# Optimization experiments

Hardware: AMD Instinct MI355X
Metric: run time of the kernel (lower is better)

Reference implementation:

```python
import jax, jax.numpy as jnp
import numpy as np

B, S, E, H = 4, 512, 512, 8
DH = E // H
HID = max(16, E // 4)  # sr_ratio=4
ALPHA = 0.1
EPS_SAFE = 0.05  # eps=1e-6 clamped to [0.05, 0.8]


def _xavier(k, shape):
    fan_out, fan_in = shape[0], shape[1]
    lim = (6.0 / (fan_in + fan_out)) ** 0.5
    return jax.random.uniform(k, shape, minval=-lim, maxval=lim, dtype=jnp.float32)


def setup_inputs() -> dict:
    key = jax.random.key(0)
    ks = jax.random.split(key, 8)
    return {
        "x": jax.random.normal(ks[0], (B, S, E), dtype=jnp.float32),
        "wq": _xavier(ks[1], (E, E)), "bq": jnp.zeros((E,), jnp.float32),
        "wk": _xavier(ks[2], (E, E)), "bk": jnp.zeros((E,), jnp.float32),
        "wv": _xavier(ks[3], (E, E)), "bv": jnp.zeros((E,), jnp.float32),
        "wo": _xavier(ks[4], (E, E)), "bo": jnp.zeros((E,), jnp.float32),
        # sr_conv1: Conv2d(1, HID, 1) -> weight [HID,1,1,1] == vector [HID]
        "w1": _xavier(ks[5], (HID, 1)).reshape(HID), "b1": jnp.zeros((HID,), jnp.float32),
        # sr_conv2: Conv2d(HID, 1, 1) -> weight [1,HID,1,1] == vector [HID]
        "w2": _xavier(ks[6], (1, HID)).reshape(HID), "b2": jnp.zeros((), jnp.float32),
    }


def _autopoietic_transform(scores, w1, b1, w2, b2):
    # scores: [B, H, S, S]
    scores = jnp.clip(jnp.nan_to_num(scores, nan=0.0, posinf=10.0, neginf=-10.0), -15.0, 15.0)
    mean_attn = scores.mean(axis=1)  # mean over heads -> [B, S, S]

    scaled = jnp.clip(jnp.clip(mean_attn, -8.0, 8.0) * EPS_SAFE, -10.0, 10.0)
    # conv1x1 (1 -> HID): broadcastmul; clamp + relu; conv1x1 (HID -> 1)
    hid = scaled[:, None, :, :] * w1[None, :, None, None] + b1[None, :, None, None]  # [B,HID,S,S]
    hid = jax.nn.relu(jnp.clip(hid, -5.0, 5.0))
    auto = jnp.einsum('bhij,h->bij', hid, w2) + b2  # [B,S,S]
    auto = jnp.clip(auto, -5.0, 5.0)

    # Taylor expansion with clamp, then sigmoid smoothing
    taylor = jnp.clip(1.0 + 0.05 * (auto * 50.0), 0.5, 1.5)
    sig = jax.nn.sigmoid(taylor)

    # fuzzy probability via entropy of softmax of mean attention
    p = jax.nn.softmax(jnp.clip(mean_attn, -10.0, 10.0), axis=-1)
    Hent = -p * jnp.log(p + 1e-6)
    Fm = jax.nn.softmax(3.0 * Hent, axis=-1)

    t = sig * Fm

    # energy (Frobenius-norm) balancing per batch
    e_o = jnp.sqrt((mean_attn ** 2).sum(axis=(1, 2))) + 1e-4
    e_t = jnp.sqrt((t ** 2).sum(axis=(1, 2))) + 1e-4
    gamma = jnp.clip(e_o / e_t, 0.8, 1.2)[:, None, None]
    t = gamma * t

    # dynamic std matching
    t_mean = t.mean(axis=(1, 2), keepdims=True)
    o_mean = mean_attn.mean(axis=(1, 2), keepdims=True)
    t_std = jnp.sqrt(jnp.clip(((t - t_mean) ** 2).mean(axis=(1, 2), keepdims=True), 0.01, None))
    o_std = jnp.sqrt(jnp.clip(((mean_attn - o_mean) ** 2).mean(axis=(1, 2), keepdims=True), 0.01, None))
    gdyn = jnp.clip(o_std / t_std, 0.8, 1.2)
    t = o_mean + gdyn * (t - t_mean)

    # residual blend of transformed map back into per-head scores (alpha=0.1), final clamp
    return jnp.clip(scores + ALPHA * t[:, None, :, :], -15.0, 15.0)


def reference(x, wq, bq, wk, bk, wv, bv, wo, bo, w1, b1, w2, b2):
    scaling = DH ** -0.5
    q = (jnp.einsum('bse,oe->bso', x, wq) + bq).reshape(B, S, H, DH).transpose(0, 2, 1, 3) * scaling
    k = (jnp.einsum('bse,oe->bso', x, wk) + bk).reshape(B, S, H, DH).transpose(0, 2, 1, 3)
    v = (jnp.einsum('bse,oe->bso', x, wv) + bv).reshape(B, S, H, DH).transpose(0, 2, 1, 3)
    scores = jnp.einsum('bhqd,bhkd->bhqk', q, k)  # [B,H,S,S]
    scores = _autopoietic_transform(scores, w1, b1, w2, b2)
    attn = jax.nn.softmax(scores, axis=-1)
    out = jnp.einsum('bhqk,bhkd->bhqd', attn, v).transpose(0, 2, 1, 3).reshape(B, S, E)
    return jnp.einsum('bse,oe->bso', out, wo) + bo
```

## Files before the change

kernel.cpp:

```cpp
#include <hip/hip_runtime.h>
#include <math.h>

#define BATCH 4
#define SEQ   512
#define EMB   512
#define NH    8
#define DHD   64
#define HIDN  128
#define ALPHA 0.1f
#define EPSS  0.05f

#define LUTN  2048
#define XMIN  (-0.4f)
#define XSTEP (0.8f / LUTN)

typedef __attribute__((ext_vector_type(8))) short  bf16x8;
typedef __attribute__((ext_vector_type(4))) float  f32x4;
#define MFMA(a,b,c) __builtin_amdgcn_mfma_f32_16x16x32_bf16((a),(b),(c),0,0,0)

__device__ __forceinline__ unsigned short f2bf(float f) {
    union { float f; unsigned u; } v; v.f = f;
    unsigned r = v.u + 0x7fffu + ((v.u >> 16) & 1u);
    return (unsigned short)(r >> 16);
}
__device__ __forceinline__ float bf2f(unsigned short h) {
    union { unsigned u; float f; } v; v.u = ((unsigned)h) << 16;
    return v.f;
}

__device__ __forceinline__ void async_lds16(const unsigned short* g, unsigned short* l) {
    __builtin_amdgcn_global_load_lds(
        (const __attribute__((address_space(1))) void*)g,
        (__attribute__((address_space(3))) void*)l, 16, 0, 0);
}

template<int KSTEPS, int UN>
__device__ __forceinline__ void gemm_core(
    const unsigned short* __restrict__ A, const unsigned short* __restrict__ B,
    int m0, int n0, unsigned short* sA, unsigned short* sB, f32x4 acc[2][4])
{
    const int K = KSTEPS * 32;
    const int tid = threadIdx.x, w = tid >> 6, lane = tid & 63;
    const int quad = lane >> 4, r = lane & 15;
    const int wm = w >> 1, wn = w & 1;
    const int lrow = lane >> 2, lc = lane & 3;
    const int sc = lc ^ (lrow & 3);
    const unsigned short* ag  = A + (long)(m0 + w * 16 + lrow) * K + sc * 8;
    const unsigned short* bg0 = B + (long)(n0 + w * 16 + lrow) * K + sc * 8;
    const unsigned short* bg1 = (UN == 4)
        ? B + (long)(n0 + (w + 4) * 16 + lrow) * K + sc * 8 : (const unsigned short*)0;
    unsigned short* dA  = sA + w * 512;
    unsigned short* dB0 = sB + w * 512;
    unsigned short* dB1 = sB + (w + 4) * 512;
    const int cs = quad ^ (r & 3);

    for (int s = 0; s < KSTEPS; s++) {
        const int k0 = s * 32;
        async_lds16(ag + k0, dA);
        async_lds16(bg0 + k0, dB0);
        if (UN == 4) async_lds16(bg1 + k0, dB1);
        __syncthreads();
        bf16x8 af[2], bf[4];
        #pragma unroll
        for (int t = 0; t < 2; t++)
            af[t] = *(const bf16x8*)(sA + (wm * 32 + t * 16 + r) * 32 + cs * 8);
        #pragma unroll
        for (int u = 0; u < UN; u++)
            bf[u] = *(const bf16x8*)(sB + (wn * UN * 16 + u * 16 + r) * 32 + cs * 8);
        #pragma unroll
        for (int t = 0; t < 2; t++)
            #pragma unroll
            for (int u = 0; u < UN; u++)
                acc[t][u] = MFMA(af[t], bf[u], acc[t][u]);
        __syncthreads();
    }
}

__global__ __launch_bounds__(256) void gemm_qkv(
    const unsigned short* __restrict__ x_ext, const unsigned short* __restrict__ w_ext,
    const float* __restrict__ bq, const float* __restrict__ bk, const float* __restrict__ bv,
    unsigned short* __restrict__ q_ext, unsigned short* __restrict__ k_ext,
    unsigned short* __restrict__ vT)
{
    __shared__ __align__(16) unsigned short sA[64 * 32];
    __shared__ __align__(16) unsigned short sB[128 * 32];
    __shared__ float sC[64 * 132];

    const int m0 = blockIdx.y * 64, n0 = blockIdx.x * 128;
    f32x4 acc[2][4] = {};
    gemm_core<48, 4>(x_ext, w_ext, m0, n0, sA, sB, acc);

    const int tid = threadIdx.x, w = tid >> 6, lane = tid & 63;
    const int quad = lane >> 4, r = lane & 15;
    const int wm = w >> 1, wn = w & 1;
    #pragma unroll
    for (int t = 0; t < 2; t++)
        #pragma unroll
        for (int u = 0; u < 4; u++)
            #pragma unroll
            for (int g = 0; g < 4; g++)
                sC[(wm * 32 + t * 16 + quad * 4 + g) * 132 + wn * 64 + u * 16 + r] = acc[t][u][g];
    __syncthreads();

    const int which = n0 >> 9;
    const int n0l = n0 & 511;
    const int h0 = n0l >> 6;
    const int b = m0 >> 9, s0 = m0 & 511;

    if (which < 2) {
        const float scl = (which == 0) ? 0.125f : 1.0f;
        const float* bias = (which == 0) ? bq : bk;
        unsigned* dst = (unsigned*)((which == 0) ? q_ext : k_ext);
        #pragma unroll
        for (int seg = 0; seg < 3; seg++) {
            const bool lo = (which == 0) ? (seg == 1) : (seg == 2);
            for (int it = 0; it < 16; it++) {
                const int idx = it * 256 + tid;
                const int row = idx >> 5;
                const int hl = row >> 6, sl = row & 63;
                const int jc = idx & 31;
                const int nc = hl * 64 + jc * 2;
                float v0 = (sC[sl * 132 + nc]     + bias[n0l + nc])     * scl;
                float v1 = (sC[sl * 132 + nc + 1] + bias[n0l + nc + 1]) * scl;
                unsigned short a0 = f2bf(v0), a1 = f2bf(v1);
                if (lo) { a0 = f2bf(v0 - bf2f(a0)); a1 = f2bf(v1 - bf2f(a1)); }
                const long orow = (long)(b * NH + h0 + hl) * SEQ + s0 + sl;
                dst[orow * 96 + seg * 32 + jc] = (unsigned)a0 | ((unsigned)a1 << 16);
            }
        }
    } else {
        unsigned* dst = (unsigned*)vT;
        for (int it = 0; it < 16; it++) {
            const int idx = it * 256 + tid;
            const int row = idx >> 5;
            const int hl = row >> 6, d = row & 63;
            const int jc = idx & 31;
            const int sl = jc * 2;
            const float bvv = bv[n0l + hl * 64 + d];
            const float v0 = sC[sl * 132 + hl * 64 + d] + bvv;
            const float v1 = sC[(sl + 1) * 132 + hl * 64 + d] + bvv;
            const long orow = (long)(b * NH + h0 + hl) * DHD + d;
            dst[orow * 256 + (s0 >> 1) + jc] = (unsigned)f2bf(v0) | ((unsigned)f2bf(v1) << 16);
        }
    }
}

__global__ __launch_bounds__(256) void gemm_scores(
    const unsigned short* __restrict__ q_ext, const unsigned short* __restrict__ k_ext,
    float* __restrict__ scores)
{
    __shared__ __align__(16) unsigned short sA[64 * 32];
    __shared__ __align__(16) unsigned short sB[128 * 32];
    const int z = blockIdx.z;
    const int m0 = blockIdx.y * 64, n0 = blockIdx.x * 128;
    f32x4 acc[2][4] = {};
    gemm_core<6, 4>(q_ext + (long)z * SEQ * 192, k_ext + (long)z * SEQ * 192,
                    m0, n0, sA, sB, acc);
    float* C = scores + (long)z * SEQ * SEQ;
    const int tid = threadIdx.x, w = tid >> 6, lane = tid & 63;
    const int quad = lane >> 4, r = lane & 15;
    const int wm = w >> 1, wn = w & 1;
    #pragma unroll
    for (int t = 0; t < 2; t++)
        #pragma unroll
        for (int u = 0; u < 4; u++)
            #pragma unroll
            for (int g = 0; g < 4; g++) {
                const int m = m0 + wm * 32 + t * 16 + quad * 4 + g;
                const int n = n0 + wn * 64 + u * 16 + r;
                C[(long)m * SEQ + n] = fminf(fmaxf(acc[t][u][g], -15.f), 15.f);
            }
}

__global__ __launch_bounds__(256) void gemm_attnv(
    const unsigned short* __restrict__ attn, const unsigned short* __restrict__ vT,
    unsigned short* __restrict__ otmp)
{
    __shared__ __align__(16) unsigned short sA[64 * 32];
    __shared__ __align__(16) unsigned short sB[64 * 32];
    __shared__ float sC[64 * 66];
    const int z = blockIdx.z;
    const int m0 = blockIdx.y * 64;
    f32x4 acc[2][4] = {};
    gemm_core<16, 2>(attn + (long)z * SEQ * SEQ, vT + (long)z * DHD * SEQ,
                     m0, 0, sA, sB, acc);
    const int tid = threadIdx.x, w = tid >> 6, lane = tid & 63;
    const int quad = lane >> 4, r = lane & 15;
    const int wm = w >> 1, wn = w & 1;
    #pragma unroll
    for (int t = 0; t < 2; t++)
        #pragma unroll
        for (int u = 0; u < 2; u++)
            #pragma unroll
            for (int g = 0; g < 4; g++)
                sC[(wm * 32 + t * 16 + quad * 4 + g) * 66 + wn * 32 + u * 16 + r] = acc[t][u][g];
    __syncthreads();
    const int b = z >> 3, h = z & 7;
    unsigned* dst = (unsigned*)otmp;
    for (int it = 0; it < 8; it++) {
        const int idx = it * 256 + tid;
        const int sr = idx >> 5, jc = idx & 31;
        const float v0 = sC[sr * 66 + jc * 2], v1 = sC[sr * 66 + jc * 2 + 1];
        dst[((long)(b * SEQ + m0 + sr)) * 256 + h * 32 + jc] =
            (unsigned)f2bf(v0) | ((unsigned)f2bf(v1) << 16);
    }
}

__global__ __launch_bounds__(256) void gemm_proj(
    const unsigned short* __restrict__ otmp, const unsigned short* __restrict__ woh,
    const float* __restrict__ bo, float* __restrict__ out)
{
    __shared__ __align__(16) unsigned short sA[64 * 32];
    __shared__ __align__(16) unsigned short sB[64 * 32];
    const int m0 = blockIdx.y * 64, n0 = blockIdx.x * 64;
    f32x4 acc[2][4] = {};
    gemm_core<16, 2>(otmp, woh, m0, n0, sA, sB, acc);
    const int tid = threadIdx.x, w = tid >> 6, lane = tid & 63;
    const int quad = lane >> 4, r = lane & 15;
    const int wm = w >> 1, wn = w & 1;
    #pragma unroll
    for (int t = 0; t < 2; t++)
        #pragma unroll
        for (int u = 0; u < 2; u++)
            #pragma unroll
            for (int g = 0; g < 4; g++) {
                const int m = m0 + wm * 32 + t * 16 + quad * 4 + g;
                const int n = n0 + wn * 32 + u * 16 + r;
                out[(long)m * EMB + n] = acc[t][u][g] + bo[n];
            }
}

__device__ __forceinline__ float blockReduceMax(float v, float* sred) {
    #pragma unroll
    for (int o = 32; o > 0; o >>= 1) v = fmaxf(v, __shfl_down(v, o));
    __syncthreads();
    if ((threadIdx.x & 63) == 0) sred[threadIdx.x >> 6] = v;
    __syncthreads();
    return fmaxf(fmaxf(sred[0], sred[1]), fmaxf(sred[2], sred[3]));
}
__device__ __forceinline__ float blockReduceSum(float v, float* sred) {
    #pragma unroll
    for (int o = 32; o > 0; o >>= 1) v += __shfl_down(v, o);
    __syncthreads();
    if ((threadIdx.x & 63) == 0) sred[threadIdx.x >> 6] = v;
    __syncthreads();
    return (sred[0] + sred[1]) + (sred[2] + sred[3]);
}

__global__ __launch_bounds__(256) void prep_kernel(
    const float* __restrict__ x,
    const float* __restrict__ wq, const float* __restrict__ wk,
    const float* __restrict__ wv, const float* __restrict__ wo,
    const float* __restrict__ w1, const float* __restrict__ b1,
    const float* __restrict__ w2, const float* __restrict__ b2,
    unsigned short* __restrict__ x_ext, unsigned short* __restrict__ w_ext,
    unsigned short* __restrict__ woh, float* __restrict__ lut)
{
    const int blk = blockIdx.x;
    if (blk < 9) {
        const int i = blk * 256 + threadIdx.x;
        if (i > LUTN) return;
        const float xv = XMIN + i * XSTEP;
        float a = 0.f;
        for (int h = 0; h < HIDN; h++) {
            float hv = xv * w1[h] + b1[h];
            hv = fminf(fmaxf(hv, -5.f), 5.f);
            hv = fmaxf(hv, 0.f);
            a += hv * w2[h];
        }
        a += b2[0];
        a = fminf(fmaxf(a, -5.f), 5.f);
        const float taylor = fminf(fmaxf(1.f + 2.5f * a, 0.5f), 1.5f);
        lut[i] = 1.f / (1.f + expf(-taylor));
        return;
    }
    const int i = (blk - 9) * 256 + threadIdx.x;
    if (i < 1048576) {
        const int m = i >> 9, k = i & 511;
        const float v = x[i];
        const unsigned short h = f2bf(v), l = f2bf(v - bf2f(h));
        const long bb = (long)m * 1536 + k;
        x_ext[bb] = h; x_ext[bb + 512] = l; x_ext[bb + 1024] = h;
    } else if (i < 1835008) {
        const int j = i - 1048576;
        const int n = j >> 9, k = j & 511;
        const float v = (j < 262144) ? wq[j] : (j < 524288 ? wk[j - 262144] : wv[j - 524288]);
        const unsigned short h = f2bf(v), l = f2bf(v - bf2f(h));
        const long bb = (long)n * 1536 + k;
        w_ext[bb] = h; w_ext[bb + 512] = h; w_ext[bb + 1024] = l;
    } else {
        const int j = i - 1835008;
        woh[j] = f2bf(wo[j]);
    }
}

__global__ __launch_bounds__(256) void transform_kernel(
    const float* __restrict__ scores,
    const float* __restrict__ lut,
    float* __restrict__ t0,
    float4* __restrict__ partials)
{
    const int r = blockIdx.x;
    const int b = r >> 9, i = r & 511;
    const int tid = threadIdx.x;

    __shared__ float slut[LUTN + 1];
    __shared__ float sred[4];

    for (int u = tid; u <= LUTN; u += 256) slut[u] = lut[u];

    const float* base = scores + (((long)(b * NH)) * SEQ + i) * SEQ;

    float mv[2], sigv[2], mclip[2];
    float lmax = -1e30f;
    __syncthreads();
    #pragma unroll
    for (int u = 0; u < 2; u++) {
        const int j = tid + u * 256;
        float s = 0.f;
        #pragma unroll
        for (int h = 0; h < NH; h++) s += base[(long)h * SEQ * SEQ + j];
        const float m = s * (1.0f / NH);
        mv[u] = m;
        const float x = fminf(fmaxf(m, -8.f), 8.f) * EPSS;
        float t = (x - XMIN) * (1.0f / XSTEP);
        int idx = (int)t;
        idx = idx < 0 ? 0 : (idx > LUTN - 1 ? LUTN - 1 : idx);
        const float frac = t - (float)idx;
        const float l0 = slut[idx], l1 = slut[idx + 1];
        sigv[u] = l0 + frac * (l1 - l0);
        const float mc = fminf(fmaxf(m, -10.f), 10.f);
        mclip[u] = mc;
        lmax = fmaxf(lmax, mc);
    }

    const float rmax = blockReduceMax(lmax, sred);
    float ex[2], lsum = 0.f;
    #pragma unroll
    for (int u = 0; u < 2; u++) { ex[u] = expf(mclip[u] - rmax); lsum += ex[u]; }
    const float rsum = blockReduceSum(lsum, sred);
    const float inv = 1.f / rsum;

    float hent[2], lmax2 = -1e30f;
    #pragma unroll
    for (int u = 0; u < 2; u++) {
        const float p = ex[u] * inv;
        const float he = -p * logf(p + 1e-6f);
        hent[u] = 3.f * he;
        lmax2 = fmaxf(lmax2, hent[u]);
    }
    const float rmax2 = blockReduceMax(lmax2, sred);
    float ex2[2], lsum2 = 0.f;
    #pragma unroll
    for (int u = 0; u < 2; u++) { ex2[u] = expf(hent[u] - rmax2); lsum2 += ex2[u]; }
    const float rsum2 = blockReduceSum(lsum2, sred);
    const float inv2 = 1.f / rsum2;

    float s_m = 0.f, s_m2 = 0.f, s_t = 0.f, s_t2 = 0.f;
    #pragma unroll
    for (int u = 0; u < 2; u++) {
        const int j = tid + u * 256;
        const float Fm = ex2[u] * inv2;
        const float tv = sigv[u] * Fm;
        t0[((long)b * SEQ + i) * SEQ + j] = tv;
        s_m += mv[u]; s_m2 += mv[u] * mv[u];
        s_t += tv;    s_t2 += tv * tv;
    }
    s_m  = blockReduceSum(s_m,  sred);
    s_m2 = blockReduceSum(s_m2, sred);
    s_t  = blockReduceSum(s_t,  sred);
    s_t2 = blockReduceSum(s_t2, sred);
    if (tid == 0) {
        partials[r] = make_float4(s_m, s_m2, s_t, s_t2);
    }
}

__global__ __launch_bounds__(256) void stats_kernel(
    const float4* __restrict__ partials, float* __restrict__ coef)
{
    const int b = blockIdx.x;
    const int tid = threadIdx.x;
    __shared__ float sred[4];

    const float4 p0 = partials[b * SEQ + tid];
    const float4 p1 = partials[b * SEQ + tid + 256];
    float sm  = p0.x + p1.x;
    float sm2 = p0.y + p1.y;
    float st  = p0.z + p1.z;
    float st2 = p0.w + p1.w;
    sm  = blockReduceSum(sm,  sred);
    sm2 = blockReduceSum(sm2, sred);
    st  = blockReduceSum(st,  sred);
    st2 = blockReduceSum(st2, sred);

    if (tid == 0) {
        const float n = (float)SEQ * (float)SEQ;
        const float e_o = sqrtf(sm2) + 1e-4f;
        const float e_t = sqrtf(st2) + 1e-4f;
        const float gamma = fminf(fmaxf(e_o / e_t, 0.8f), 1.2f);
        const float o_mean = sm / n, t0m = st / n;
        const float o_var = fmaxf(sm2 / n - o_mean * o_mean, 0.f);
        const float o_std = sqrtf(fmaxf(o_var, 0.01f));
        const float t0var = fmaxf(st2 / n - t0m * t0m, 0.f);
        const float t_std = sqrtf(fmaxf(gamma * gamma * t0var, 0.01f));
        const float gdyn = fminf(fmaxf(o_std / t_std, 0.8f), 1.2f);
        const float c1 = gdyn * gamma;
        coef[b] = o_mean - c1 * t0m;
        coef[BATCH + b] = c1;
    }
}

__global__ __launch_bounds__(256) void softmax_kernel(
    const float* __restrict__ scores,
    const float* __restrict__ t0,
    const float* __restrict__ coef,
    unsigned short* __restrict__ attn)
{
    const int r = blockIdx.x;
    const int i = r & 511;
    const int bh = r >> 9;
    const int b = bh >> 3;
    const float c0 = coef[b], c1 = coef[BATCH + b];
    const float* row = scores + (long)r * SEQ;
    const float* trow = t0 + ((long)b * SEQ + i) * SEQ;
    const int tid = threadIdx.x;
    __shared__ float sred[4];

    float v[2], lmax = -1e30f;
    #pragma unroll
    for (int u = 0; u < 2; u++) {
        const int j = tid + u * 256;
        float sv = row[j] + ALPHA * (c0 + c1 * trow[j]);
        sv = fminf(fmaxf(sv, -15.f), 15.f);
        v[u] = sv;
        lmax = fmaxf(lmax, sv);
    }
    const float rmax = blockReduceMax(lmax, sred);
    float ex[2], lsum = 0.f;
    #pragma unroll
    for (int u = 0; u < 2; u++) { ex[u] = expf(v[u] - rmax); lsum += ex[u]; }
    const float rsum = blockReduceSum(lsum, sred);
    const float inv = 1.f / rsum;
    #pragma unroll
    for (int u = 0; u < 2; u++)
        attn[(long)r * SEQ + tid + u * 256] = f2bf(ex[u] * inv);
}

extern "C" void kernel_launch(void* const* d_in, const int* in_sizes, int n_in,
                              void* d_out, int out_size, void* d_ws, size_t ws_size,
                              hipStream_t stream) {
    const float* x  = (const float*)d_in[0];
    const float* wq = (const float*)d_in[1];
    const float* bq = (const float*)d_in[2];
    const float* wk = (const float*)d_in[3];
    const float* bk = (const float*)d_in[4];
    const float* wv = (const float*)d_in[5];
    const float* bv = (const float*)d_in[6];
    const float* wo = (const float*)d_in[7];
    const float* bo = (const float*)d_in[8];
    const float* w1 = (const float*)d_in[9];
    const float* b1 = (const float*)d_in[10];
    const float* w2 = (const float*)d_in[11];
    const float* b2 = (const float*)d_in[12];
    float* out = (float*)d_out;

    char* wsb = (char*)d_ws;
    float*  scores   = (float*)wsb;
    float*  t0       = scores + 8388608;
    float4* partials = (float4*)(t0 + 1048576);
    float*  coef     = (float*)(partials + 2048);
    float*  lutbuf   = coef + 8;
    unsigned short* u16 = (unsigned short*)(wsb + (40u << 20));
    unsigned short* x_ext = u16;
    unsigned short* w_ext = x_ext + 3145728;
    unsigned short* q_ext = w_ext + 2359296;
    unsigned short* attn  = u16;
    unsigned short* k_ext = q_ext + 3145728;
    unsigned short* vT    = k_ext + 3145728;
    unsigned short* otmp  = vT + 1048576;
    unsigned short* woh   = otmp + 1048576;

    prep_kernel<<<dim3(9 + 8192), dim3(256), 0, stream>>>(
        x, wq, wk, wv, wo, w1, b1, w2, b2, x_ext, w_ext, woh, lutbuf);

    gemm_qkv<<<dim3(12, 32), dim3(256), 0, stream>>>(
        x_ext, w_ext, bq, bk, bv, q_ext, k_ext, vT);

    gemm_scores<<<dim3(4, 8, 32), dim3(256), 0, stream>>>(q_ext, k_ext, scores);

    transform_kernel<<<dim3(BATCH * SEQ), dim3(256), 0, stream>>>(
        scores, lutbuf, t0, partials);

    stats_kernel<<<dim3(BATCH), dim3(256), 0, stream>>>(partials, coef);

    softmax_kernel<<<dim3(BATCH * NH * SEQ), dim3(256), 0, stream>>>(
        scores, t0, coef, attn);

    gemm_attnv<<<dim3(1, 8, 32), dim3(256), 0, stream>>>(attn, vT, otmp);

    gemm_proj<<<dim3(8, 32), dim3(256), 0, stream>>>(otmp, woh, bo, out);
}
```

Baseline: 174.9 us.

## Fuse stats, softmax and attn@V into one kernel; narrow QKV GEMM tiles

Merges the per-batch stats reduction, row softmax, and the attention-times-V GEMM into one kernel. Each block redundantly recomputes the batch coefficients from the partials, softmaxes 32 rows into LDS as bf16, then runs the MFMA product against V from LDS. This removes the bf16 attention matrix round trip through global memory and two kernel launches. The QKV GEMM also moves to 64-wide N tiles, doubling its grid so more blocks run in parallel. The cost is redundant stats work per block and a serial softmax/GEMM phase with little overlap.

```diff
diff --git a/kernel.cpp b/kernel.cpp
--- a/kernel.cpp
+++ b/kernel.cpp
@@ -83,12 +83,12 @@
     unsigned short* __restrict__ vT)
 {
     __shared__ __align__(16) unsigned short sA[64 * 32];
-    __shared__ __align__(16) unsigned short sB[128 * 32];
-    __shared__ float sC[64 * 132];
-
-    const int m0 = blockIdx.y * 64, n0 = blockIdx.x * 128;
+    __shared__ __align__(16) unsigned short sB[64 * 32];
+    __shared__ float sC[64 * 68];
+
+    const int m0 = blockIdx.y * 64, n0 = blockIdx.x * 64;
     f32x4 acc[2][4] = {};
-    gemm_core<48, 4>(x_ext, w_ext, m0, n0, sA, sB, acc);
+    gemm_core<48, 2>(x_ext, w_ext, m0, n0, sA, sB, acc);
 
     const int tid = threadIdx.x, w = tid >> 6, lane = tid & 63;
     const int quad = lane >> 4, r = lane & 15;
@@ -96,10 +96,10 @@
     #pragma unroll
     for (int t = 0; t < 2; t++)
         #pragma unroll
-        for (int u = 0; u < 4; u++)
+        for (int u = 0; u < 2; u++)
             #pragma unroll
             for (int g = 0; g < 4; g++)
-                sC[(wm * 32 + t * 16 + quad * 4 + g) * 132 + wn * 64 + u * 16 + r] = acc[t][u][g];
+                sC[(wm * 32 + t * 16 + quad * 4 + g) * 68 + wn * 32 + u * 16 + r] = acc[t][u][g];
     __syncthreads();
 
     const int which = n0 >> 9;
@@ -114,32 +114,32 @@
         #pragma unroll
         for (int seg = 0; seg < 3; seg++) {
             const bool lo = (which == 0) ? (seg == 1) : (seg == 2);
-            for (int it = 0; it < 16; it++) {
+            #pragma unroll
+            for (int it = 0; it < 8; it++) {
                 const int idx = it * 256 + tid;
-                const int row = idx >> 5;
-                const int hl = row >> 6, sl = row & 63;
+                const int sl = idx >> 5;
                 const int jc = idx & 31;
-                const int nc = hl * 64 + jc * 2;
-                float v0 = (sC[sl * 132 + nc]     + bias[n0l + nc])     * scl;
-                float v1 = (sC[sl * 132 + nc + 1] + bias[n0l + nc + 1]) * scl;
+                const int nc = jc * 2;
+                float v0 = (sC[sl * 68 + nc]     + bias[n0l + nc])     * scl;
+                float v1 = (sC[sl * 68 + nc + 1] + bias[n0l + nc + 1]) * scl;
                 unsigned short a0 = f2bf(v0), a1 = f2bf(v1);
                 if (lo) { a0 = f2bf(v0 - bf2f(a0)); a1 = f2bf(v1 - bf2f(a1)); }
-                const long orow = (long)(b * NH + h0 + hl) * SEQ + s0 + sl;
+                const long orow = (long)(b * NH + h0) * SEQ + s0 + sl;
                 dst[orow * 96 + seg * 32 + jc] = (unsigned)a0 | ((unsigned)a1 << 16);
             }
         }
     } else {
         unsigned* dst = (unsigned*)vT;
-        for (int it = 0; it < 16; it++) {
+        #pragma unroll
+        for (int it = 0; it < 8; it++) {
             const int idx = it * 256 + tid;
-            const int row = idx >> 5;
-            const int hl = row >> 6, d = row & 63;
+            const int d = idx >> 5;
             const int jc = idx & 31;
             const int sl = jc * 2;
-            const float bvv = bv[n0l + hl * 64 + d];
-            const float v0 = sC[sl * 132 + hl * 64 + d] + bvv;
-            const float v1 = sC[(sl + 1) * 132 + hl * 64 + d] + bvv;
-            const long orow = (long)(b * NH + h0 + hl) * DHD + d;
+            const float bvv = bv[n0l + d];
+            const float v0 = sC[sl * 68 + d] + bvv;
+            const float v1 = sC[(sl + 1) * 68 + d] + bvv;
+            const long orow = (long)(b * NH + h0) * DHD + d;
             dst[orow * 256 + (s0 >> 1) + jc] = (unsigned)f2bf(v0) | ((unsigned)f2bf(v1) << 16);
         }
     }
@@ -172,40 +172,6 @@
             }
 }
 
-__global__ __launch_bounds__(256) void gemm_attnv(
-    const unsigned short* __restrict__ attn, const unsigned short* __restrict__ vT,
-    unsigned short* __restrict__ otmp)
-{
-    __shared__ __align__(16) unsigned short sA[64 * 32];
-    __shared__ __align__(16) unsigned short sB[64 * 32];
-    __shared__ float sC[64 * 66];
-    const int z = blockIdx.z;
-    const int m0 = blockIdx.y * 64;
-    f32x4 acc[2][4] = {};
-    gemm_core<16, 2>(attn + (long)z * SEQ * SEQ, vT + (long)z * DHD * SEQ,
-                     m0, 0, sA, sB, acc);
-    const int tid = threadIdx.x, w = tid >> 6, lane = tid & 63;
-    const int quad = lane >> 4, r = lane & 15;
-    const int wm = w >> 1, wn = w & 1;
-    #pragma unroll
-    for (int t = 0; t < 2; t++)
-        #pragma unroll
-        for (int u = 0; u < 2; u++)
-            #pragma unroll
-            for (int g = 0; g < 4; g++)
-                sC[(wm * 32 + t * 16 + quad * 4 + g) * 66 + wn * 32 + u * 16 + r] = acc[t][u][g];
-    __syncthreads();
-    const int b = z >> 3, h = z & 7;
-    unsigned* dst = (unsigned*)otmp;
-    for (int it = 0; it < 8; it++) {
-        const int idx = it * 256 + tid;
-        const int sr = idx >> 5, jc = idx & 31;
-        const float v0 = sC[sr * 66 + jc * 2], v1 = sC[sr * 66 + jc * 2 + 1];
-        dst[((long)(b * SEQ + m0 + sr)) * 256 + h * 32 + jc] =
-            (unsigned)f2bf(v0) | ((unsigned)f2bf(v1) << 16);
-    }
-}
-
 __global__ __launch_bounds__(256) void gemm_proj(
     const unsigned short* __restrict__ otmp, const unsigned short* __restrict__ woh,
     const float* __restrict__ bo, float* __restrict__ out)
@@ -230,6 +196,14 @@
             }
 }
 
+__device__ __forceinline__ float blockReduceSum(float v, float* sred) {
+    #pragma unroll
+    for (int o = 32; o > 0; o >>= 1) v += __shfl_down(v, o);
+    __syncthreads();
+    if ((threadIdx.x & 63) == 0) sred[threadIdx.x >> 6] = v;
+    __syncthreads();
+    return (sred[0] + sred[1]) + (sred[2] + sred[3]);
+}
 __device__ __forceinline__ float blockReduceMax(float v, float* sred) {
     #pragma unroll
     for (int o = 32; o > 0; o >>= 1) v = fmaxf(v, __shfl_down(v, o));
@@ -237,14 +211,6 @@
     if ((threadIdx.x & 63) == 0) sred[threadIdx.x >> 6] = v;
     __syncthreads();
     return fmaxf(fmaxf(sred[0], sred[1]), fmaxf(sred[2], sred[3]));
-}
-__device__ __forceinline__ float blockReduceSum(float v, float* sred) {
-    #pragma unroll
-    for (int o = 32; o > 0; o >>= 1) v += __shfl_down(v, o);
-    __syncthreads();
-    if ((threadIdx.x & 63) == 0) sred[threadIdx.x >> 6] = v;
-    __syncthreads();
-    return (sred[0] + sred[1]) + (sred[2] + sred[3]);
 }
 
 __global__ __launch_bounds__(256) void prep_kernel(
@@ -375,75 +341,106 @@
     }
 }
 
-__global__ __launch_bounds__(256) void stats_kernel(
-    const float4* __restrict__ partials, float* __restrict__ coef)
-{
-    const int b = blockIdx.x;
-    const int tid = threadIdx.x;
+__global__ __launch_bounds__(256) void softmax_attnv(
+    const float* __restrict__ scores,
+    const float* __restrict__ t0,
+    const float4* __restrict__ partials,
+    const unsigned short* __restrict__ vT,
+    unsigned short* __restrict__ otmp)
+{
+    __shared__ __align__(16) unsigned short attnS[32 * 520];
+    __shared__ __align__(16) unsigned short sB[64 * 32];
+    __shared__ float sC[32 * 66];
     __shared__ float sred[4];
+
+    const int m0 = blockIdx.x * 32;
+    const int z  = blockIdx.y;
+    const int b  = z >> 3, h = z & 7;
+    const int tid = threadIdx.x, wv = tid >> 6, lane = tid & 63;
 
     const float4 p0 = partials[b * SEQ + tid];
     const float4 p1 = partials[b * SEQ + tid + 256];
-    float sm  = p0.x + p1.x;
-    float sm2 = p0.y + p1.y;
-    float st  = p0.z + p1.z;
-    float st2 = p0.w + p1.w;
-    sm  = blockReduceSum(sm,  sred);
-    sm2 = blockReduceSum(sm2, sred);
-    st  = blockReduceSum(st,  sred);
-    st2 = blockReduceSum(st2, sred);
-
-    if (tid == 0) {
-        const float n = (float)SEQ * (float)SEQ;
-        const float e_o = sqrtf(sm2) + 1e-4f;
-        const float e_t = sqrtf(st2) + 1e-4f;
-        const float gamma = fminf(fmaxf(e_o / e_t, 0.8f), 1.2f);
-        const float o_mean = sm / n, t0m = st / n;
-        const float o_var = fmaxf(sm2 / n - o_mean * o_mean, 0.f);
-        const float o_std = sqrtf(fmaxf(o_var, 0.01f));
-        const float t0var = fmaxf(st2 / n - t0m * t0m, 0.f);
-        const float t_std = sqrtf(fmaxf(gamma * gamma * t0var, 0.01f));
-        const float gdyn = fminf(fmaxf(o_std / t_std, 0.8f), 1.2f);
-        const float c1 = gdyn * gamma;
-        coef[b] = o_mean - c1 * t0m;
-        coef[BATCH + b] = c1;
-    }
-}
-
-__global__ __launch_bounds__(256) void softmax_kernel(
-    const float* __restrict__ scores,
-    const float* __restrict__ t0,
-    const float* __restrict__ coef,
-    unsigned short* __restrict__ attn)
-{
-    const int r = blockIdx.x;
-    const int i = r & 511;
-    const int bh = r >> 9;
-    const int b = bh >> 3;
-    const float c0 = coef[b], c1 = coef[BATCH + b];
-    const float* row = scores + (long)r * SEQ;
-    const float* trow = t0 + ((long)b * SEQ + i) * SEQ;
-    const int tid = threadIdx.x;
-    __shared__ float sred[4];
-
-    float v[2], lmax = -1e30f;
-    #pragma unroll
-    for (int u = 0; u < 2; u++) {
-        const int j = tid + u * 256;
-        float sv = row[j] + ALPHA * (c0 + c1 * trow[j]);
-        sv = fminf(fmaxf(sv, -15.f), 15.f);
-        v[u] = sv;
-        lmax = fmaxf(lmax, sv);
-    }
-    const float rmax = blockReduceMax(lmax, sred);
-    float ex[2], lsum = 0.f;
-    #pragma unroll
-    for (int u = 0; u < 2; u++) { ex[u] = expf(v[u] - rmax); lsum += ex[u]; }
-    const float rsum = blockReduceSum(lsum, sred);
-    const float inv = 1.f / rsum;
+    float sm  = blockReduceSum(p0.x + p1.x, sred);
+    float sm2 = blockReduceSum(p0.y + p1.y, sred);
+    float st  = blockReduceSum(p0.z + p1.z, sred);
+    float st2 = blockReduceSum(p0.w + p1.w, sred);
+    const float n = (float)SEQ * (float)SEQ;
+    const float gamma = fminf(fmaxf((sqrtf(sm2) + 1e-4f) / (sqrtf(st2) + 1e-4f), 0.8f), 1.2f);
+    const float o_mean = sm / n, t0m = st / n;
+    const float o_std = sqrtf(fmaxf(fmaxf(sm2 / n - o_mean * o_mean, 0.f), 0.01f));
+    const float t_std = sqrtf(fmaxf(gamma * gamma * fmaxf(st2 / n - t0m * t0m, 0.f), 0.01f));
+    const float gdyn = fminf(fmaxf(o_std / t_std, 0.8f), 1.2f);
+    const float c1 = gdyn * gamma;
+    const float c0 = o_mean - c1 * t0m;
+
+    const int j0 = lane * 8;
+    for (int it = 0; it < 8; it++) {
+        const int rowl = it * 4 + wv;
+        const float* srow = scores + ((long)z * SEQ + m0 + rowl) * SEQ + j0;
+        const float* trow = t0 + ((long)b * SEQ + m0 + rowl) * SEQ + j0;
+        const float4 s0 = ((const float4*)srow)[0], s1 = ((const float4*)srow)[1];
+        const float4 tt0 = ((const float4*)trow)[0], tt1 = ((const float4*)trow)[1];
+        float sv[8] = { s0.x, s0.y, s0.z, s0.w, s1.x, s1.y, s1.z, s1.w };
+        const float tvv[8] = { tt0.x, tt0.y, tt0.z, tt0.w, tt1.x, tt1.y, tt1.z, tt1.w };
+        float lmax = -1e30f;
+        #pragma unroll
+        for (int u = 0; u < 8; u++) {
+            float s = sv[u] + ALPHA * (c0 + c1 * tvv[u]);
+            s = fminf(fmaxf(s, -15.f), 15.f);
+            sv[u] = s;
+            lmax = fmaxf(lmax, s);
+        }
+        #pragma unroll
+        for (int o = 32; o > 0; o >>= 1) lmax = fmaxf(lmax, __shfl_down(lmax, o));
+        lmax = __shfl(lmax, 0);
+        float lsum = 0.f;
+        #pragma unroll
+        for (int u = 0; u < 8; u++) { sv[u] = expf(sv[u] - lmax); lsum += sv[u]; }
+        #pragma unroll
+        for (int o = 32; o > 0; o >>= 1) lsum += __shfl_down(lsum, o);
+        lsum = __shfl(lsum, 0);
+        const float inv = 1.f / lsum;
+        bf16x8 pk;
+        #pragma unroll
+        for (int u = 0; u < 8; u++) pk[u] = (short)f2bf(sv[u] * inv);
+        *(bf16x8*)(attnS + rowl * 520 + j0) = pk;
+    }
+    __syncthreads();
+
+    const int quad = lane >> 4, r = lane & 15;
+    const int wm = wv >> 1, wn = wv & 1;
+    const int lrow = lane >> 2, lc = lane & 3;
+    const int sc = lc ^ (lrow & 3);
+    const int cs = quad ^ (r & 3);
+    const unsigned short* bg = vT + (long)z * DHD * SEQ + (long)(wv * 16 + lrow) * SEQ + sc * 8;
+    unsigned short* dB = sB + wv * 512;
+    f32x4 acc[2] = {};
+    for (int kc = 0; kc < 16; kc++) {
+        async_lds16(bg + kc * 32, dB);
+        __syncthreads();
+        const bf16x8 a = *(const bf16x8*)(attnS + (wm * 16 + r) * 520 + kc * 32 + quad * 8);
+        const bf16x8 b0 = *(const bf16x8*)(sB + (wn * 32 + r) * 32 + cs * 8);
+        const bf16x8 b1 = *(const bf16x8*)(sB + (wn * 32 + 16 + r) * 32 + cs * 8);
+        acc[0] = MFMA(a, b0, acc[0]);
+        acc[1] = MFMA(a, b1, acc[1]);
+        __syncthreads();
+    }
+
     #pragma unroll
     for (int u = 0; u < 2; u++)
-        attn[(long)r * SEQ + tid + u * 256] = f2bf(ex[u] * inv);
+        #pragma unroll
+        for (int g = 0; g < 4; g++)
+            sC[(wm * 16 + quad * 4 + g) * 66 + wn * 32 + u * 16 + r] = acc[u][g];
+    __syncthreads();
+    unsigned* dst = (unsigned*)otmp;
+    #pragma unroll
+    for (int it = 0; it < 4; it++) {
+        const int idx = it * 256 + tid;
+        const int sr = idx >> 5, jc = idx & 31;
+        const float v0 = sC[sr * 66 + jc * 2], v1 = sC[sr * 66 + jc * 2 + 1];
+        dst[((long)(b * SEQ + m0 + sr)) * 256 + h * 32 + jc] =
+            (unsigned)f2bf(v0) | ((unsigned)f2bf(v1) << 16);
+    }
 }
 
 extern "C" void kernel_launch(void* const* d_in, const int* in_sizes, int n_in,
@@ -468,13 +465,11 @@
     float*  scores   = (float*)wsb;
     float*  t0       = scores + 8388608;
     float4* partials = (float4*)(t0 + 1048576);
-    float*  coef     = (float*)(partials + 2048);
-    float*  lutbuf   = coef + 8;
+    float*  lutbuf   = (float*)(partials + 2048);
     unsigned short* u16 = (unsigned short*)(wsb + (40u << 20));
     unsigned short* x_ext = u16;
     unsigned short* w_ext = x_ext + 3145728;
     unsigned short* q_ext = w_ext + 2359296;
-    unsigned short* attn  = u16;
     unsigned short* k_ext = q_ext + 3145728;
     unsigned short* vT    = k_ext + 3145728;
     unsigned short* otmp  = vT + 1048576;
@@ -483,7 +478,7 @@
     prep_kernel<<<dim3(9 + 8192), dim3(256), 0, stream>>>(
         x, wq, wk, wv, wo, w1, b1, w2, b2, x_ext, w_ext, woh, lutbuf);
 
-    gemm_qkv<<<dim3(12, 32), dim3(256), 0, stream>>>(
+    gemm_qkv<<<dim3(24, 32), dim3(256), 0, stream>>>(
         x_ext, w_ext, bq, bk, bv, q_ext, k_ext, vT);
 
     gemm_scores<<<dim3(4, 8, 32), dim3(256), 0, stream>>>(q_ext, k_ext, scores);
@@ -491,12 +486,8 @@
     transform_kernel<<<dim3(BATCH * SEQ), dim3(256), 0, stream>>>(
         scores, lutbuf, t0, partials);
 
-    stats_kernel<<<dim3(BATCH), dim3(256), 0, stream>>>(partials, coef);
-
-    softmax_kernel<<<dim3(BATCH * NH * SEQ), dim3(256), 0, stream>>>(
-        scores, t0, coef, attn);
-
-    gemm_attnv<<<dim3(1, 8, 32), dim3(256), 0, stream>>>(attn, vT, otmp);
+    softmax_attnv<<<dim3(16, 32), dim3(256), 0, stream>>>(
+        scores, t0, partials, vT, otmp);
 
     gemm_proj<<<dim3(8, 32), dim3(256), 0, stream>>>(otmp, woh, bo, out);
 }
```

Measured after the change: 164.4 us. 1.06x faster.
